# Kernel optimization log

Hardware: AMD Instinct MI355X
Metric: run time of the kernel (lower is better)

## Reference

```python
import jax, jax.numpy as jnp
import numpy as np

EPS = 1e-5


def setup_inputs() -> dict:
    key = jax.random.key(0)
    k1, k2 = jax.random.split(key)
    B, C, D, H, W = 2, 8, 128, 192, 192
    inp = jax.random.normal(k1, (B, C, D, H, W), dtype=jnp.float32)
    tgt = jax.random.randint(k2, (B, 1, D, H, W), 0, C, dtype=jnp.int32)
    return {"input": inp, "target": tgt, "background": 0}


def reference(input, target, background):
    # input: [B, C, D, H, W] logits; target: [B, 1, D, H, W] class indices.
    B, C = input.shape[0], input.shape[1]
    pred = jnp.argmax(input, axis=1).reshape(B, -1)            # [B, N] int
    tgt = target.reshape(B, -1).astype(pred.dtype)             # [B, N]
    # Instead of materializing two [B, C, N] one-hot tensors (as the torch
    # code does via scatter_), accumulate a per-batch confusion histogram:
    # comb = tgt * C + pred, counts -> conf[b, t, p].
    comb = tgt * C + pred                                      # [B, N]
    conf = jax.vmap(lambda c: jnp.bincount(c, length=C * C))(comb)
    conf = conf.reshape(B, C, C).astype(jnp.float32)           # [B, Ctgt, Cpred]
    tp = jnp.diagonal(conf, axis1=1, axis2=2)                  # [B, C]
    psum = conf.sum(axis=1)                                    # pred counts [B, C]
    tsum = conf.sum(axis=2)                                    # target counts [B, C]
    if not background:
        tp, psum, tsum = tp[:, 1:], psum[:, 1:], tsum[:, 1:]
    dice = 2.0 * tp / (psum + tsum + EPS)
    return dice, tp, psum, tsum
```

## Files before the change

kernel.cpp:

```cpp
#include <hip/hip_runtime.h>

typedef float f32x4 __attribute__((ext_vector_type(4)));
typedef int   i32x4 __attribute__((ext_vector_type(4)));


template <int CT>
__global__ __launch_bounds__(256, 6)
void conf_hist_kernel(const float* __restrict__ inp,
                      const int* __restrict__ tgt,
                      unsigned int* __restrict__ conf,
                      int Crt, long long N) {
    const int C = (CT > 0) ? CT : Crt;
    __shared__ unsigned int sh[64];
    const int cc = C * C;
    for (int i = threadIdx.x; i < cc; i += blockDim.x) sh[i] = 0u;
    __syncthreads();

    const int b = blockIdx.y;
    const long long Nv4 = N >> 2;
    const f32x4* __restrict__ ip = (const f32x4*)(inp + (long long)b * C * N);
    const i32x4* __restrict__ tq = (const i32x4*)(tgt + (long long)b * N);

    const long long stride = (long long)gridDim.x * blockDim.x;
    for (long long i = (long long)blockIdx.x * blockDim.x + threadIdx.x;
         i < Nv4; i += stride) {
        f32x4 best = __builtin_nontemporal_load(ip + i);
        int bx = 0, by = 0, bz = 0, bw = 0;
        #pragma unroll
        for (int c = 1; c < ((CT > 0) ? CT : 8); ++c) {
            if (CT == 0 && c >= C) break;
            f32x4 v = __builtin_nontemporal_load(ip + (long long)c * Nv4 + i);
            if (v.x > best.x) { best.x = v.x; bx = c; }
            if (v.y > best.y) { best.y = v.y; by = c; }
            if (v.z > best.z) { best.z = v.z; bz = c; }
            if (v.w > best.w) { best.w = v.w; bw = c; }
        }
        i32x4 t = __builtin_nontemporal_load(tq + i);
        atomicAdd(&sh[t.x * C + bx], 1u);
        atomicAdd(&sh[t.y * C + by], 1u);
        atomicAdd(&sh[t.z * C + bz], 1u);
        atomicAdd(&sh[t.w * C + bw], 1u);
    }

    const long long tail0 = Nv4 << 2;
    if (tail0 < N && blockIdx.x == 0) {
        const float* p = (const float*)ip;
        for (long long e = tail0 + threadIdx.x; e < N; e += blockDim.x) {
            float bv = p[e];
            int bc = 0;
            for (int c = 1; c < C; ++c) {
                float v = p[(long long)c * N + e];
                if (v > bv) { bv = v; bc = c; }
            }
            int t = ((const int*)tq)[e];
            atomicAdd(&sh[t * C + bc], 1u);
        }
    }

    __syncthreads();
    unsigned int* cb = conf + b * cc;
    for (int i = threadIdx.x; i < cc; i += blockDim.x) {
        unsigned int v = sh[i];
        if (v) atomicAdd(&cb[i], v);
    }
}

__global__ void finalize_kernel(const unsigned int* __restrict__ conf,
                                float* __restrict__ out,
                                int B, int C, int ncls) {
    int tid = threadIdx.x;
    if (tid >= B * C) return;
    int b = tid / C;
    int k = tid % C;
    const unsigned int* cb = conf + b * C * C;

    float tp = (float)cb[k * C + k];
    float tsum = 0.0f, psum = 0.0f;
    for (int j = 0; j < C; ++j) {
        tsum += (float)cb[k * C + j];
        psum += (float)cb[j * C + k];
    }
    int off = C - ncls;
    if (k >= off) {
        int idx = b * ncls + (k - off);
        int s = B * ncls;
        float dice = 2.0f * tp / (psum + tsum + 1e-5f);
        out[idx]         = dice;
        out[s + idx]     = tp;
        out[2 * s + idx] = psum;
        out[3 * s + idx] = tsum;
    }
}

extern "C" void kernel_launch(void* const* d_in, const int* in_sizes, int n_in,
                              void* d_out, int out_size, void* d_ws, size_t ws_size,
                              hipStream_t stream) {
    const float* inp = (const float*)d_in[0];
    const int* tgt = (const int*)d_in[1];
    float* out = (float*)d_out;
    unsigned int* conf = (unsigned int*)d_ws;

    const int C = in_sizes[0] / in_sizes[1];
    int ncls, B;
    if (C > 1 && out_size % (4 * (C - 1)) == 0 &&
        in_sizes[1] % (out_size / (4 * (C - 1))) == 0) {
        ncls = C - 1;
        B = out_size / (4 * (C - 1));
    } else {
        ncls = C;
        B = out_size / (4 * C);
    }
    const long long N = (long long)in_sizes[1] / B;
    const long long Nv4 = N >> 2;

    hipMemsetAsync(conf, 0, (size_t)(B * C * C) * sizeof(unsigned int), stream);

    const int block = 256;
    long long bx = (Nv4 + (long long)block * 6 - 1) / ((long long)block * 6);
    if (bx < 1) bx = 1;
    if (bx > 4096) bx = 4096;
    dim3 grid((unsigned)bx, (unsigned)B);

    if (C == 8)
        conf_hist_kernel<8><<<grid, block, 0, stream>>>(inp, tgt, conf, C, N);
    else
        conf_hist_kernel<0><<<grid, block, 0, stream>>>(inp, tgt, conf, C, N);

    finalize_kernel<<<1, 64, 0, stream>>>(conf, out, B, C, ncls);
}
```

Baseline: 71.31 us.

## Replace global atomics and memset with per-block partial histograms reduced in finalize

```diff
diff --git a/kernel.cpp b/kernel.cpp
--- a/kernel.cpp
+++ b/kernel.cpp
@@ -8,11 +8,11 @@
 __global__ __launch_bounds__(256, 6)
 void conf_hist_kernel(const float* __restrict__ inp,
                       const int* __restrict__ tgt,
-                      unsigned int* __restrict__ conf,
-                      int Crt, long long N) {
+                      unsigned int* __restrict__ partial,
+                      int Crt, long long N, int nbx) {
     const int C = (CT > 0) ? CT : Crt;
-    __shared__ unsigned int sh[64];
     const int cc = C * C;
+    __shared__ unsigned int sh[256];
     for (int i = threadIdx.x; i < cc; i += blockDim.x) sh[i] = 0u;
     __syncthreads();
 
@@ -21,9 +21,12 @@
     const f32x4* __restrict__ ip = (const f32x4*)(inp + (long long)b * C * N);
     const i32x4* __restrict__ tq = (const i32x4*)(tgt + (long long)b * N);
 
-    const long long stride = (long long)gridDim.x * blockDim.x;
-    for (long long i = (long long)blockIdx.x * blockDim.x + threadIdx.x;
-         i < Nv4; i += stride) {
+    const long long stride = (long long)nbx * blockDim.x;
+    const long long i0 = (long long)blockIdx.x * blockDim.x + threadIdx.x;
+    const long long nit = Nv4 / stride;
+    const long long rem = Nv4 - nit * stride;
+
+    auto body = [&](long long i) {
         f32x4 best = __builtin_nontemporal_load(ip + i);
         int bx = 0, by = 0, bz = 0, bw = 0;
         #pragma unroll
@@ -40,7 +43,11 @@
         atomicAdd(&sh[t.y * C + by], 1u);
         atomicAdd(&sh[t.z * C + bz], 1u);
         atomicAdd(&sh[t.w * C + bw], 1u);
-    }
+    };
+
+    long long i = i0;
+    for (long long k = 0; k < nit; ++k, i += stride) body(i);
+    if (i0 < rem) body(i);
 
     const long long tail0 = Nv4 << 2;
     if (tail0 < N && blockIdx.x == 0) {
@@ -58,37 +65,54 @@
     }
 
     __syncthreads();
-    unsigned int* cb = conf + b * cc;
-    for (int i = threadIdx.x; i < cc; i += blockDim.x) {
-        unsigned int v = sh[i];
-        if (v) atomicAdd(&cb[i], v);
-    }
+    for (int bin = threadIdx.x; bin < cc; bin += blockDim.x)
+        partial[(long long)(b * cc + bin) * nbx + blockIdx.x] = sh[bin];
 }
 
-__global__ void finalize_kernel(const unsigned int* __restrict__ conf,
+__global__ void finalize_kernel(const unsigned int* __restrict__ partial,
                                 float* __restrict__ out,
-                                int B, int C, int ncls) {
-    int tid = threadIdx.x;
-    if (tid >= B * C) return;
-    int b = tid / C;
-    int k = tid % C;
-    const unsigned int* cb = conf + b * C * C;
+                                int B, int C, int ncls, int nbx) {
+    const int cc = C * C;
+    const int bins = B * cc;
+    __shared__ unsigned int conf[1024];
+    const int tid = threadIdx.x;
 
-    float tp = (float)cb[k * C + k];
-    float tsum = 0.0f, psum = 0.0f;
-    for (int j = 0; j < C; ++j) {
-        tsum += (float)cb[k * C + j];
-        psum += (float)cb[j * C + k];
+    for (int bin = tid; bin < bins; bin += blockDim.x) {
+        const unsigned int* row = partial + (long long)bin * nbx;
+        unsigned int acc = 0;
+        if ((nbx & 3) == 0) {
+            const uint4* r4 = (const uint4*)row;
+            for (int q = 0; q < (nbx >> 2); ++q) {
+                uint4 v = r4[q];
+                acc += v.x + v.y + v.z + v.w;
+            }
+        } else {
+            for (int k = 0; k < nbx; ++k) acc += row[k];
+        }
+        conf[bin] = acc;
     }
-    int off = C - ncls;
-    if (k >= off) {
-        int idx = b * ncls + (k - off);
-        int s = B * ncls;
-        float dice = 2.0f * tp / (psum + tsum + 1e-5f);
-        out[idx]         = dice;
-        out[s + idx]     = tp;
-        out[2 * s + idx] = psum;
-        out[3 * s + idx] = tsum;
+    __syncthreads();
+
+    if (tid < B * C) {
+        int b = tid / C;
+        int k = tid % C;
+        const unsigned int* cb = conf + b * cc;
+        float tp = (float)cb[k * C + k];
+        float tsum = 0.0f, psum = 0.0f;
+        for (int j = 0; j < C; ++j) {
+            tsum += (float)cb[k * C + j];
+            psum += (float)cb[j * C + k];
+        }
+        int off = C - ncls;
+        if (k >= off) {
+            int idx = b * ncls + (k - off);
+            int s = B * ncls;
+            float dice = 2.0f * tp / (psum + tsum + 1e-5f);
+            out[idx]         = dice;
+            out[s + idx]     = tp;
+            out[2 * s + idx] = psum;
+            out[3 * s + idx] = tsum;
+        }
     }
 }
 
@@ -98,7 +122,7 @@
     const float* inp = (const float*)d_in[0];
     const int* tgt = (const int*)d_in[1];
     float* out = (float*)d_out;
-    unsigned int* conf = (unsigned int*)d_ws;
+    unsigned int* partial = (unsigned int*)d_ws;
 
     const int C = in_sizes[0] / in_sizes[1];
     int ncls, B;
@@ -112,19 +136,21 @@
     }
     const long long N = (long long)in_sizes[1] / B;
     const long long Nv4 = N >> 2;
-
-    hipMemsetAsync(conf, 0, (size_t)(B * C * C) * sizeof(unsigned int), stream);
+    const int cc = C * C;
 
     const int block = 256;
     long long bx = (Nv4 + (long long)block * 6 - 1) / ((long long)block * 6);
     if (bx < 1) bx = 1;
     if (bx > 4096) bx = 4096;
-    dim3 grid((unsigned)bx, (unsigned)B);
+    long long bx_cap = (long long)(ws_size / ((size_t)B * cc * sizeof(unsigned int)));
+    if (bx > bx_cap) bx = bx_cap < 1 ? 1 : bx_cap;
+    const int nbx = (int)bx;
+    dim3 grid((unsigned)nbx, (unsigned)B);
 
     if (C == 8)
-        conf_hist_kernel<8><<<grid, block, 0, stream>>>(inp, tgt, conf, C, N);
+        conf_hist_kernel<8><<<grid, block, 0, stream>>>(inp, tgt, partial, C, N, nbx);
     else
-        conf_hist_kernel<0><<<grid, block, 0, stream>>>(inp, tgt, conf, C, N);
+        conf_hist_kernel<0><<<grid, block, 0, stream>>>(inp, tgt, partial, C, N, nbx);
 
-    finalize_kernel<<<1, 64, 0, stream>>>(conf, out, B, C, ncls);
+    finalize_kernel<<<1, 256, 0, stream>>>(partial, out, B, C, ncls, nbx);
 }
```

Result: slower. 79.91 us (+12.1%).
